# Kernel tuning notes

Hardware: AMD Instinct MI355X
Metric: run time of the kernel (lower is better)

The kernel has to match this reference:

```python
import jax, jax.numpy as jnp
import numpy as np

B, T, D, H = 4096, 512, 25, 25
NUM_LAYERS = 3


def setup_inputs() -> dict:
    key = jax.random.key(0)
    ks = jax.random.split(key, 9)
    s = 1.0 / np.sqrt(H)  # torch LSTM/Linear default init scale
    return {
        "x": jax.random.normal(ks[0], (B, T, D), dtype=jnp.float32),
        "Wih": jax.random.uniform(ks[1], (NUM_LAYERS, 4 * H, D), minval=-s, maxval=s),
        "Whh": jax.random.uniform(ks[2], (NUM_LAYERS, 4 * H, H), minval=-s, maxval=s),
        "bih": jax.random.uniform(ks[3], (NUM_LAYERS, 4 * H), minval=-s, maxval=s),
        "bhh": jax.random.uniform(ks[4], (NUM_LAYERS, 4 * H), minval=-s, maxval=s),
        "W1": jax.random.uniform(ks[5], (16, H), minval=-s, maxval=s),
        "b1": jax.random.uniform(ks[6], (16,), minval=-s, maxval=s),
        "W2": jax.random.uniform(ks[7], (14, 16), minval=-0.25, maxval=0.25),
        "b2": jax.random.uniform(ks[8], (14,), minval=-0.25, maxval=0.25),
    }


def _lstm_layer(x, Wih, Whh, b):
    """Single LSTM layer, batch_first. x: [B,T,Din] -> hs: [B,T,H].
    Torch gate order: i, f, g, o."""
    # Precompute input contribution for all timesteps at once: [B,T,4H]
    xg = jnp.einsum('btd,gd->btg', x, Wih) + b

    def step(carry, xg_t):
        h, c = carry
        g = xg_t + h @ Whh.T  # [B,4H]
        i, f, gg, o = jnp.split(g, 4, axis=-1)
        c = jax.nn.sigmoid(f) * c + jax.nn.sigmoid(i) * jnp.tanh(gg)
        h = jax.nn.sigmoid(o) * jnp.tanh(c)
        return (h, c), h

    h0 = jnp.zeros((x.shape[0], H), x.dtype)
    (_, _), hs = jax.lax.scan(step, (h0, h0), jnp.swapaxes(xg, 0, 1))  # [T,B,H]
    return jnp.swapaxes(hs, 0, 1)


def reference(x, Wih, Whh, bih, bhh, W1, b1, W2, b2):
    h = x
    for l in range(NUM_LAYERS):  # eval mode: inter-layer dropout disabled
        h = _lstm_layer(h, Wih[l], Whh[l], bih[l] + bhh[l])
    last = h[:, -1, :]                       # [B,H]
    out = jax.nn.relu(last @ W1.T + b1)      # [B,16]
    return jax.nn.softmax(out @ W2.T + b2, axis=1)  # [B,14]
```

## Files before the change

### kernel.cpp

```cpp
#include <hip/hip_runtime.h>


typedef float f32x2 __attribute__((ext_vector_type(2)));
typedef float f32x4 __attribute__((ext_vector_type(4)));

#define NT 512
#define ND 25

__device__ __forceinline__ float exp2f_(float x) { return __builtin_amdgcn_exp2f(x); }
__device__ __forceinline__ float rcpf_(float x)  { return __builtin_amdgcn_rcpf(x); }
__device__ __forceinline__ float tanhfast(float x) {
    float s = rcpf_(1.f + exp2f_(-2.885390082f * x));
    return fmaf(2.f, s, -1.f);
}
__device__ __forceinline__ float rdlane(float v, int i) {
    return __uint_as_float(__builtin_amdgcn_readlane(__float_as_uint(v), i));
}
__device__ __forceinline__ void pkfma(f32x2& a, f32x2 w, f32x2 v) {
    asm("v_pk_fma_f32 %0, %1, %2, %0" : "+v"(a) : "v"(w), "v"(v));
}
#define LO2(v) __builtin_shufflevector(v, v, 0, 1)
#define HI2(v) __builtin_shufflevector(v, v, 2, 3)

#define WXDECL  f32x2 wx0  = {wihp[0],  wihp[1]},  wx1  = {wihp[2],  wihp[3]},  \
                      wx2  = {wihp[4],  wihp[5]},  wx3  = {wihp[6],  wihp[7]},  \
                      wx4  = {wihp[8],  wihp[9]},  wx5  = {wihp[10], wihp[11]}, \
                      wx6  = {wihp[12], wihp[13]}, wx7  = {wihp[14], wihp[15]}, \
                      wx8  = {wihp[16], wihp[17]}, wx9  = {wihp[18], wihp[19]}, \
                      wx10 = {wihp[20], wihp[21]}, wx11 = {wihp[22], wihp[23]}, \
                      wx12 = {wihp[24], 0.f};
#define WHDECL  float wh0  = whhp[0],  wh1  = whhp[1],  wh2  = whhp[2],  \
                      wh3  = whhp[3],  wh4  = whhp[4],  wh5  = whhp[5],  \
                      wh6  = whhp[6],  wh7  = whhp[7],  wh8  = whhp[8],  \
                      wh9  = whhp[9],  wh10 = whhp[10], wh11 = whhp[11], \
                      wh12 = whhp[12], wh13 = whhp[13], wh14 = whhp[14], \
                      wh15 = whhp[15], wh16 = whhp[16], wh17 = whhp[17], \
                      wh18 = whhp[18], wh19 = whhp[19], wh20 = whhp[20], \
                      wh21 = whhp[21], wh22 = whhp[22], wh23 = whhp[23], \
                      wh24 = whhp[24];
#define HT(d, A) A = fmaf(wh##d, rdlane(hreg, d), A);

__global__ __launch_bounds__(256, 3)
void lstm6(const float* __restrict__ xin,
           const float* __restrict__ Wih,
           const float* __restrict__ Whh,
           const float* __restrict__ bih,
           const float* __restrict__ bhh,
           const float* __restrict__ W1,
           const float* __restrict__ b1,
           const float* __restrict__ W2,
           const float* __restrict__ b2,
           float* __restrict__ out,
           float* __restrict__ ws)
{
    __shared__ __align__(16) float xb[2][2][28];
    __shared__ __align__(16) float act4[2][2][25][4];

    const int wid  = threadIdx.x >> 6;
    const int lane = threadIdx.x & 63;
    const int wb   = wid >> 1;
    const int role = wid & 1;
    const int b    = (blockIdx.x << 1) + wb;

    const int lrow = (lane < 50) ? lane : 49;

    const int ul   = (lrow >= ND) ? lrow - ND : lrow;
    const int slot = role * 2 + (lrow >= ND ? 1 : 0);
    float* const actw0 = &act4[wb][0][ul][slot];
    float* const actw1 = &act4[wb][1][ul][slot];
    const int ur = (lane < ND) ? lane : ND - 1;
    const f32x4* const actr0 = (const f32x4*)&act4[wb][0][ur][0];
    const f32x4* const actr1 = (const f32x4*)&act4[wb][1][ur][0];
    const f32x4* const xr0 = (const f32x4*)&xb[wb][0][0];
    const f32x4* const xr1 = (const f32x4*)&xb[wb][1][0];
    float* const xw0 = &xb[wb][0][lane < ND ? lane : 0];
    float* const xw1 = &xb[wb][1][lane < ND ? lane : 0];

    const bool  isg    = (role == 1) && (lane < ND);
    const float emul   = isg ? -2.885390082f : -1.442695041f;
    const float ascale = isg ?  2.0f : 1.0f;
    const float abias  = isg ? -1.0f : 0.0f;

    float hreg = 0.f;

#pragma unroll
    for (int l = 0; l < 3; ++l) {
        const int row = l * 100 + role * 50 + lrow;
        const float* wihp = Wih + row * ND;
        const float* whhp = Whh + row * ND;
        WXDECL
        WHDECL
        const float bias = bih[row] + bhh[row];

        const float* src = (l == 0) ? (xin + (size_t)b * NT * ND)
                                    : (ws  + (size_t)b * NT * ND);
        float* wsrow = ws + (size_t)b * NT * ND;

        __syncthreads();
        if (role == 1) {
            if (lane < ND)       xb[wb][0][lane] = src[lane];
            else if (lane < 28) { xb[wb][0][lane] = 0.f; xb[wb][1][lane] = 0.f; }
        }
        float c = 0.f;
        hreg = 0.f;
        float xnext = (role == 1 && lane < ND) ? src[ND + lane] : 0.f;
        __syncthreads();

        for (int t = 0; t < NT; ++t) {
            const int p = t & 1;
            const f32x4* const xr = p ? xr1 : xr0;

            const f32x4 v0 = xr[0], v1 = xr[1], v2 = xr[2], v3 = xr[3];
            const f32x4 v4 = xr[4], v5 = xr[5], v6 = xr[6];
            f32x2 A0 = {bias, 0.f}, A1 = {0.f, 0.f}, A2 = {0.f, 0.f}, A3 = {0.f, 0.f};
            pkfma(A0, wx0,  LO2(v0)); pkfma(A1, wx1,  HI2(v0));
            pkfma(A2, wx2,  LO2(v1)); pkfma(A3, wx3,  HI2(v1));
            pkfma(A0, wx4,  LO2(v2)); pkfma(A1, wx5,  HI2(v2));
            pkfma(A2, wx6,  LO2(v3)); pkfma(A3, wx7,  HI2(v3));
            pkfma(A0, wx8,  LO2(v4)); pkfma(A1, wx9,  HI2(v4));
            pkfma(A2, wx10, LO2(v5)); pkfma(A3, wx11, HI2(v5));
            pkfma(A0, wx12, LO2(v6));

            float b0 = 0.f, b1r = 0.f, b2r = 0.f, b3 = 0.f;
            HT(0,  b0) HT(1,  b1r) HT(2,  b2r) HT(3,  b3)
            HT(4,  b0) HT(5,  b1r) HT(6,  b2r) HT(7,  b3)
            HT(8,  b0) HT(9,  b1r) HT(10, b2r) HT(11, b3)
            HT(12, b0) HT(13, b1r) HT(14, b2r) HT(15, b3)
            HT(16, b0) HT(17, b1r) HT(18, b2r) HT(19, b3)
            HT(20, b0) HT(21, b1r) HT(22, b2r) HT(23, b3)
            HT(24, b0)

            f32x2 S = A0 + A1; S += A2; S += A3;
            const float acc = (S.x + S.y) + ((b0 + b1r) + (b2r + b3));

            const float a = fmaf(ascale, rcpf_(1.f + exp2f_(emul * acc)), abias);
            if (lane < 50) *(p ? actw1 : actw0) = a;

            if (role == 1 && lane < ND) {
                *(p ? xw0 : xw1) = xnext;
                if (t + 2 < NT) xnext = src[(size_t)(t + 2) * ND + lane];
            }

            asm volatile("s_waitcnt lgkmcnt(0)\n\ts_barrier" ::: "memory");

            const f32x4 q = p ? *actr1 : *actr0;
            c = fmaf(q.y, c, q.x * q.z);
            hreg = q.w * tanhfast(c);
            if (role == 0 && lane < ND && l < 2) wsrow[(size_t)t * ND + lane] = hreg;
        }
    }

    {
        const int hl = (lane < 16) ? lane : 15;
        float u = b1[hl];
#pragma unroll
        for (int d = 0; d < ND; ++d)
            u = fmaf(W1[hl * ND + d], rdlane(hreg, d), u);
        u = fmaxf(u, 0.f);

        const int cl = (lane < 14) ? lane : 13;
        float lg = b2[cl];
#pragma unroll
        for (int r = 0; r < 16; ++r)
            lg = fmaf(W2[cl * 16 + r], rdlane(u, r), lg);

        float m = -1e30f;
#pragma unroll
        for (int j = 0; j < 14; ++j) m = fmaxf(m, rdlane(lg, j));
        float sum = 0.f;
#pragma unroll
        for (int j = 0; j < 14; ++j)
            sum += exp2f_(1.442695041f * (rdlane(lg, j) - m));
        const float p = exp2f_(1.442695041f * (lg - m)) * rcpf_(sum);
        if (role == 0 && lane < 14) out[b * 14 + lane] = p;
    }
}

extern "C" void kernel_launch(void* const* d_in, const int* in_sizes, int n_in,
                              void* d_out, int out_size, void* d_ws, size_t ws_size,
                              hipStream_t stream)
{
    const float* x   = (const float*)d_in[0];
    const float* Wih = (const float*)d_in[1];
    const float* Whh = (const float*)d_in[2];
    const float* bih = (const float*)d_in[3];
    const float* bhh = (const float*)d_in[4];
    const float* W1  = (const float*)d_in[5];
    const float* b1  = (const float*)d_in[6];
    const float* W2  = (const float*)d_in[7];
    const float* b2  = (const float*)d_in[8];
    float* outp = (float*)d_out;
    float* ws   = (float*)d_ws;

    dim3 grid(4096 / 2), block(256);
    hipLaunchKernelGGL(lstm6, grid, block, 0, stream,
                       x, Wih, Whh, bih, bhh, W1, b1, W2, b2, outp, ws);
}
```

Baseline: 2.166 ms.

## Wavefront-pipeline the three LSTM layers concurrently within one block via LDS

Instead of running the three layers one after another per batch row and spilling hidden states to global workspace, each block now holds one batch row with three wave pairs, one per layer. The pairs run in a skewed pipeline where layer l processes timestep s-l and passes h through shared memory to the next layer. The recurrent matvec now reads h from LDS and uses packed FMAs instead of readlane, which removes the global workspace traffic. The cost is two barriers per step, three extra pipeline steps, and a different occupancy (384 threads, one batch row per block).

```diff
diff --git a/kernel.cpp b/kernel.cpp
--- a/kernel.cpp
+++ b/kernel.cpp
@@ -21,27 +21,10 @@
 }
 #define LO2(v) __builtin_shufflevector(v, v, 0, 1)
 #define HI2(v) __builtin_shufflevector(v, v, 2, 3)
+#define LDSBAR() asm volatile("s_waitcnt lgkmcnt(0)\n\ts_barrier" ::: "memory")
 
-#define WXDECL  f32x2 wx0  = {wihp[0],  wihp[1]},  wx1  = {wihp[2],  wihp[3]},  \
-                      wx2  = {wihp[4],  wihp[5]},  wx3  = {wihp[6],  wihp[7]},  \
-                      wx4  = {wihp[8],  wihp[9]},  wx5  = {wihp[10], wihp[11]}, \
-                      wx6  = {wihp[12], wihp[13]}, wx7  = {wihp[14], wihp[15]}, \
-                      wx8  = {wihp[16], wihp[17]}, wx9  = {wihp[18], wihp[19]}, \
-                      wx10 = {wihp[20], wihp[21]}, wx11 = {wihp[22], wihp[23]}, \
-                      wx12 = {wihp[24], 0.f};
-#define WHDECL  float wh0  = whhp[0],  wh1  = whhp[1],  wh2  = whhp[2],  \
-                      wh3  = whhp[3],  wh4  = whhp[4],  wh5  = whhp[5],  \
-                      wh6  = whhp[6],  wh7  = whhp[7],  wh8  = whhp[8],  \
-                      wh9  = whhp[9],  wh10 = whhp[10], wh11 = whhp[11], \
-                      wh12 = whhp[12], wh13 = whhp[13], wh14 = whhp[14], \
-                      wh15 = whhp[15], wh16 = whhp[16], wh17 = whhp[17], \
-                      wh18 = whhp[18], wh19 = whhp[19], wh20 = whhp[20], \
-                      wh21 = whhp[21], wh22 = whhp[22], wh23 = whhp[23], \
-                      wh24 = whhp[24];
-#define HT(d, A) A = fmaf(wh##d, rdlane(hreg, d), A);
-
-__global__ __launch_bounds__(256, 3)
-void lstm6(const float* __restrict__ xin,
+__global__ __launch_bounds__(384, 4)
+void lstm7(const float* __restrict__ xin,
            const float* __restrict__ Wih,
            const float* __restrict__ Whh,
            const float* __restrict__ bih,
@@ -50,107 +33,111 @@
            const float* __restrict__ b1,
            const float* __restrict__ W2,
            const float* __restrict__ b2,
-           float* __restrict__ out,
-           float* __restrict__ ws)
+           float* __restrict__ out)
 {
-    __shared__ __align__(16) float xb[2][2][28];
-    __shared__ __align__(16) float act4[2][2][25][4];
+    __shared__ __align__(16) float vec[3][2][56];
+    __shared__ __align__(16) float act4[3][2][25][4];
 
     const int wid  = threadIdx.x >> 6;
     const int lane = threadIdx.x & 63;
-    const int wb   = wid >> 1;
+    const int l    = wid >> 1;
     const int role = wid & 1;
-    const int b    = (blockIdx.x << 1) + wb;
+    const int b    = blockIdx.x;
 
     const int lrow = (lane < 50) ? lane : 49;
+    const int row  = l * 100 + role * 50 + lrow;
+    const float* wihp = Wih + row * ND;
+    const float* whhp = Whh + row * ND;
 
-    const int ul   = (lrow >= ND) ? lrow - ND : lrow;
-    const int slot = role * 2 + (lrow >= ND ? 1 : 0);
-    float* const actw0 = &act4[wb][0][ul][slot];
-    float* const actw1 = &act4[wb][1][ul][slot];
-    const int ur = (lane < ND) ? lane : ND - 1;
-    const f32x4* const actr0 = (const f32x4*)&act4[wb][0][ur][0];
-    const f32x4* const actr1 = (const f32x4*)&act4[wb][1][ur][0];
-    const f32x4* const xr0 = (const f32x4*)&xb[wb][0][0];
-    const f32x4* const xr1 = (const f32x4*)&xb[wb][1][0];
-    float* const xw0 = &xb[wb][0][lane < ND ? lane : 0];
-    float* const xw1 = &xb[wb][1][lane < ND ? lane : 0];
+    f32x2 wp0  = {wihp[0],  wihp[1]},  wp1  = {wihp[2],  wihp[3]};
+    f32x2 wp2  = {wihp[4],  wihp[5]},  wp3  = {wihp[6],  wihp[7]};
+    f32x2 wp4  = {wihp[8],  wihp[9]},  wp5  = {wihp[10], wihp[11]};
+    f32x2 wp6  = {wihp[12], wihp[13]}, wp7  = {wihp[14], wihp[15]};
+    f32x2 wp8  = {wihp[16], wihp[17]}, wp9  = {wihp[18], wihp[19]};
+    f32x2 wp10 = {wihp[20], wihp[21]}, wp11 = {wihp[22], wihp[23]};
+    f32x2 wp12 = {wihp[24], 0.f};
+    f32x2 wp13 = {whhp[0],  whhp[1]},  wp14 = {whhp[2],  whhp[3]};
+    f32x2 wp15 = {whhp[4],  whhp[5]},  wp16 = {whhp[6],  whhp[7]};
+    f32x2 wp17 = {whhp[8],  whhp[9]},  wp18 = {whhp[10], whhp[11]};
+    f32x2 wp19 = {whhp[12], whhp[13]}, wp20 = {whhp[14], whhp[15]};
+    f32x2 wp21 = {whhp[16], whhp[17]}, wp22 = {whhp[18], whhp[19]};
+    f32x2 wp23 = {whhp[20], whhp[21]}, wp24 = {whhp[22], whhp[23]};
+    f32x2 wp25 = {whhp[24], 0.f};
+    const float bias = bih[row] + bhh[row];
 
     const bool  isg    = (role == 1) && (lane < ND);
     const float emul   = isg ? -2.885390082f : -1.442695041f;
     const float ascale = isg ?  2.0f : 1.0f;
     const float abias  = isg ? -1.0f : 0.0f;
 
-    float hreg = 0.f;
+    const int ul   = (lrow >= ND) ? lrow - ND : lrow;
+    const int slot = role * 2 + (lrow >= ND ? 1 : 0);
+    const int uu   = (lane < ND) ? lane : ND - 1;
 
-#pragma unroll
-    for (int l = 0; l < 3; ++l) {
-        const int row = l * 100 + role * 50 + lrow;
-        const float* wihp = Wih + row * ND;
-        const float* whhp = Whh + row * ND;
-        WXDECL
-        WHDECL
-        const float bias = bih[row] + bhh[row];
+    if (threadIdx.x < 3 * 2 * 56) ((float*)vec)[threadIdx.x] = 0.f;
+    __syncthreads();
 
-        const float* src = (l == 0) ? (xin + (size_t)b * NT * ND)
-                                    : (ws  + (size_t)b * NT * ND);
-        float* wsrow = ws + (size_t)b * NT * ND;
+    const float* srcx = xin + (size_t)b * NT * ND;
+    const bool stager = (l == 0) && (role == 1) && (lane < ND);
+    float xv_cur = 0.f, xv_nxt = 0.f;
+    if (stager) { xv_cur = srcx[lane]; xv_nxt = srcx[ND + lane]; }
 
-        __syncthreads();
-        if (role == 1) {
-            if (lane < ND)       xb[wb][0][lane] = src[lane];
-            else if (lane < 28) { xb[wb][0][lane] = 0.f; xb[wb][1][lane] = 0.f; }
+    float c = 0.f, hreg = 0.f;
+
+    for (int s = 0; s < NT + 3; ++s) {
+        const int p = s & 1;
+        const int t = s - l;
+        float* const vp = &vec[l][p][0];
+
+        if (role == 0) {
+            if (t >= 1 && t <= NT) {
+                const f32x4 q = *(const f32x4*)&act4[l][p ^ 1][uu][0];
+                c = fmaf(q.y, c, q.x * q.z);
+                hreg = q.w * tanhfast(c);
+                if (lane < ND) {
+                    vp[26 + lane] = hreg;
+                    if (l < 2) vec[l + 1][p][lane] = hreg;
+                }
+            }
+        } else if (l == 0) {
+            if (lane < ND && s < NT) {
+                vp[lane] = xv_cur;
+                xv_cur = xv_nxt;
+                if (s + 2 < NT) xv_nxt = srcx[(size_t)(s + 2) * ND + lane];
+            }
         }
-        float c = 0.f;
-        hreg = 0.f;
-        float xnext = (role == 1 && lane < ND) ? src[ND + lane] : 0.f;
-        __syncthreads();
+        LDSBAR();
 
-        for (int t = 0; t < NT; ++t) {
-            const int p = t & 1;
-            const f32x4* const xr = p ? xr1 : xr0;
-
-            const f32x4 v0 = xr[0], v1 = xr[1], v2 = xr[2], v3 = xr[3];
-            const f32x4 v4 = xr[4], v5 = xr[5], v6 = xr[6];
+        if (t >= 0 && t < NT) {
+            const f32x4* const vv = (const f32x4*)vp;
+            const f32x4 v0 = vv[0],  v1 = vv[1],  v2 = vv[2],  v3 = vv[3];
+            const f32x4 v4 = vv[4],  v5 = vv[5],  v6 = vv[6],  v7 = vv[7];
+            const f32x4 v8 = vv[8],  v9 = vv[9],  v10 = vv[10], v11 = vv[11];
+            const f32x4 v12 = vv[12];
             f32x2 A0 = {bias, 0.f}, A1 = {0.f, 0.f}, A2 = {0.f, 0.f}, A3 = {0.f, 0.f};
-            pkfma(A0, wx0,  LO2(v0)); pkfma(A1, wx1,  HI2(v0));
-            pkfma(A2, wx2,  LO2(v1)); pkfma(A3, wx3,  HI2(v1));
-            pkfma(A0, wx4,  LO2(v2)); pkfma(A1, wx5,  HI2(v2));
-            pkfma(A2, wx6,  LO2(v3)); pkfma(A3, wx7,  HI2(v3));
-            pkfma(A0, wx8,  LO2(v4)); pkfma(A1, wx9,  HI2(v4));
-            pkfma(A2, wx10, LO2(v5)); pkfma(A3, wx11, HI2(v5));
-            pkfma(A0, wx12, LO2(v6));
-
-            float b0 = 0.f, b1r = 0.f, b2r = 0.f, b3 = 0.f;
-            HT(0,  b0) HT(1,  b1r) HT(2,  b2r) HT(3,  b3)
-            HT(4,  b0) HT(5,  b1r) HT(6,  b2r) HT(7,  b3)
-            HT(8,  b0) HT(9,  b1r) HT(10, b2r) HT(11, b3)
-            HT(12, b0) HT(13, b1r) HT(14, b2r) HT(15, b3)
-            HT(16, b0) HT(17, b1r) HT(18, b2r) HT(19, b3)
-            HT(20, b0) HT(21, b1r) HT(22, b2r) HT(23, b3)
-            HT(24, b0)
-
-            f32x2 S = A0 + A1; S += A2; S += A3;
-            const float acc = (S.x + S.y) + ((b0 + b1r) + (b2r + b3));
+            pkfma(A0, wp0,  LO2(v0));  pkfma(A1, wp1,  HI2(v0));
+            pkfma(A2, wp2,  LO2(v1));  pkfma(A3, wp3,  HI2(v1));
+            pkfma(A0, wp4,  LO2(v2));  pkfma(A1, wp5,  HI2(v2));
+            pkfma(A2, wp6,  LO2(v3));  pkfma(A3, wp7,  HI2(v3));
+            pkfma(A0, wp8,  LO2(v4));  pkfma(A1, wp9,  HI2(v4));
+            pkfma(A2, wp10, LO2(v5));  pkfma(A3, wp11, HI2(v5));
+            pkfma(A0, wp12, LO2(v6));  pkfma(A1, wp13, HI2(v6));
+            pkfma(A2, wp14, LO2(v7));  pkfma(A3, wp15, HI2(v7));
+            pkfma(A0, wp16, LO2(v8));  pkfma(A1, wp17, HI2(v8));
+            pkfma(A2, wp18, LO2(v9));  pkfma(A3, wp19, HI2(v9));
+            pkfma(A0, wp20, LO2(v10)); pkfma(A1, wp21, HI2(v10));
+            pkfma(A2, wp22, LO2(v11)); pkfma(A3, wp23, HI2(v11));
+            pkfma(A0, wp24, LO2(v12)); pkfma(A1, wp25, HI2(v12));
+            A0 = A0 + A1; A2 = A2 + A3; A0 = A0 + A2;
+            const float acc = A0.x + A0.y;
 
             const float a = fmaf(ascale, rcpf_(1.f + exp2f_(emul * acc)), abias);
-            if (lane < 50) *(p ? actw1 : actw0) = a;
-
-            if (role == 1 && lane < ND) {
-                *(p ? xw0 : xw1) = xnext;
-                if (t + 2 < NT) xnext = src[(size_t)(t + 2) * ND + lane];
-            }
-
-            asm volatile("s_waitcnt lgkmcnt(0)\n\ts_barrier" ::: "memory");
-
-            const f32x4 q = p ? *actr1 : *actr0;
-            c = fmaf(q.y, c, q.x * q.z);
-            hreg = q.w * tanhfast(c);
-            if (role == 0 && lane < ND && l < 2) wsrow[(size_t)t * ND + lane] = hreg;
+            if (lane < 50) act4[l][p][ul][slot] = a;
         }
+        LDSBAR();
     }
 
-    {
+    if (l == 2 && role == 0) {
         const int hl = (lane < 16) ? lane : 15;
         float u = b1[hl];
 #pragma unroll
@@ -171,8 +158,8 @@
 #pragma unroll
         for (int j = 0; j < 14; ++j)
             sum += exp2f_(1.442695041f * (rdlane(lg, j) - m));
-        const float p = exp2f_(1.442695041f * (lg - m)) * rcpf_(sum);
-        if (role == 0 && lane < 14) out[b * 14 + lane] = p;
+        const float pr = exp2f_(1.442695041f * (lg - m)) * rcpf_(sum);
+        if (lane < 14) out[b * 14 + lane] = pr;
     }
 }
 
@@ -190,9 +177,9 @@
     const float* W2  = (const float*)d_in[7];
     const float* b2  = (const float*)d_in[8];
     float* outp = (float*)d_out;
-    float* ws   = (float*)d_ws;
+    (void)d_ws; (void)ws_size;
 
-    dim3 grid(4096 / 2), block(256);
-    hipLaunchKernelGGL(lstm6, grid, block, 0, stream,
-                       x, Wih, Whh, bih, bhh, W1, b1, W2, b2, outp, ws);
+    dim3 grid(4096), block(384);
+    hipLaunchKernelGGL(lstm7, grid, block, 0, stream,
+                       x, Wih, Whh, bih, bhh, W1, b1, W2, b2, outp);
 }
```

New measurement: 2.899 ms. +33.8%, slower.
